# Optimization experiments

Hardware: AMD Instinct MI355X
Metric: run time of the kernel (lower is better)

The kernel has to match this reference:

```python
import jax, jax.numpy as jnp
import numpy as np

N, E, F, ED, L = 50000, 800000, 64, 16, 2
EPS_BN = 1e-5


def setup_inputs() -> dict:
    key = jax.random.key(0)
    ks = jax.random.split(key, 8)
    s = 0.05
    return {
        "x": jax.random.normal(ks[0], (N, F), jnp.float32),
        "edge_index": jax.random.randint(ks[1], (2, E), 0, N),
        "edge_attr": jax.random.normal(ks[2], (E, ED), jnp.float32),
        # per-layer stacked params (L layers)
        "We": jax.random.normal(ks[3], (L, ED, F), jnp.float32) * s,
        "be": jnp.zeros((L, F), jnp.float32),
        "Wpre": jax.random.normal(ks[4], (L, 2 * F, F), jnp.float32) * s,
        "bpre": jnp.zeros((L, F), jnp.float32),
        "Wpost": jax.random.normal(ks[5], (L, 7 * F, F), jnp.float32) * s,
        "bpost": jnp.zeros((L, F), jnp.float32),
        "Wlin": jax.random.normal(ks[6], (L, F, F), jnp.float32) * s,
        "blin": jnp.zeros((L, F), jnp.float32),
        "gamma": jnp.ones((L, F), jnp.float32),
        "beta": jnp.zeros((L, F), jnp.float32),
    }


def _layer(x, src, dst, edge_attr, We, be, Wpre, bpre, Wpost, bpost, Wlin, blin, gamma, beta):
    # message: edge encoder + pre-MLP on cat(x_j, e)   [E, F]
    e = edge_attr @ We + be
    h = jnp.concatenate([x[src], e], axis=-1) @ Wpre + bpre
    # multi-aggregator segment reduce to target nodes (index = dst)
    cnt = jax.ops.segment_sum(jnp.ones(h.shape[0], h.dtype), dst, num_segments=N)
    safe_cnt = jnp.maximum(cnt, 1.0)
    mean = jax.ops.segment_sum(h, dst, num_segments=N) / safe_cnt[:, None]
    empty = (cnt == 0)[:, None]
    mn = jnp.where(empty, 0.0, jax.ops.segment_min(h, dst, num_segments=N))
    mx = jnp.where(empty, 0.0, jax.ops.segment_max(h, dst, num_segments=N))
    agg = jnp.concatenate([mean, mn, mx], axis=-1)  # [N, 3F]
    # scalers: identity, then amplification (deg=None => avg from bincount of degrees)
    deg_i = cnt.astype(jnp.int32)
    bc = jnp.bincount(deg_i, length=N).astype(h.dtype)
    avg_log = jnp.mean(jnp.log(bc + 1.0))
    amp = (jnp.log(safe_cnt + 1.0) / avg_log)[:, None]
    out = jnp.concatenate([agg, agg * amp], axis=-1)  # [N, 6F]
    # post-MLP on cat(x, aggregated), final linear
    out = jnp.concatenate([x, out], axis=-1) @ Wpost + bpost  # [N, F]
    out = out @ Wlin + blin
    # BatchNorm1d (batch stats, biased var) + ReLU
    mu = out.mean(axis=0)
    var = jnp.mean((out - mu) ** 2, axis=0)
    out = gamma * (out - mu) / jnp.sqrt(var + EPS_BN) + beta
    return jax.nn.relu(out)


def reference(x, edge_index, edge_attr, We, be, Wpre, bpre, Wpost, bpost, Wlin, blin, gamma, beta):
    src, dst = edge_index[0], edge_index[1]
    for l in range(L):
        x = _layer(x, src, dst, edge_attr, We[l], be[l], Wpre[l], bpre[l],
                   Wpost[l], bpost[l], Wlin[l], blin[l], gamma[l], beta[l])
    return x
```

## Files before the change

kernel.cpp:

```cpp
#include <hip/hip_runtime.h>
#include <math.h>

static constexpr int NN = 50000;
static constexpr long NE = 800000;
static constexpr int FF = 64;
static constexpr int EDIM = 16;
static constexpr int NLAYER = 2;
static constexpr float EPSBN = 1e-5f;
static constexpr int NGRP = NN / 16;
static constexpr int SCB = 512;
static constexpr int NSCB = (NN + SCB - 1) / SCB;

typedef __attribute__((ext_vector_type(8))) short short8v;
typedef __attribute__((ext_vector_type(4))) float f32x4;

#define MFMA16(a, b, c) __builtin_amdgcn_mfma_f32_16x16x32_bf16(a, b, c, 0, 0, 0)

__device__ __forceinline__ short f2bf(float f) {
    unsigned u = __float_as_uint(f);
    unsigned r = u + 0x7FFFu + ((u >> 16) & 1u);
    return (short)(r >> 16);
}
__device__ __forceinline__ float bf2f(unsigned short h) {
    return __uint_as_float(((unsigned)h) << 16);
}
__device__ __forceinline__ unsigned pk2(float lo, float hi) {
    return (unsigned)(unsigned short)f2bf(lo) | ((unsigned)(unsigned short)f2bf(hi) << 16);
}
__device__ __forceinline__ short8v pack8(const float* p) {
    const float4* q = (const float4*)p;
    float4 a = q[0], b = q[1];
    short8v v;
    v[0] = f2bf(a.x); v[1] = f2bf(a.y); v[2] = f2bf(a.z); v[3] = f2bf(a.w);
    v[4] = f2bf(b.x); v[5] = f2bf(b.y); v[6] = f2bf(b.z); v[7] = f2bf(b.w);
    return v;
}
__device__ __forceinline__ void pack8s(const float* p, short8v& hi, short8v& lo) {
    const float4* q = (const float4*)p;
    float4 a = q[0], b = q[1];
    float v[8] = {a.x, a.y, a.z, a.w, b.x, b.y, b.z, b.w};
#pragma unroll
    for (int j = 0; j < 8; ++j) {
        short h = f2bf(v[j]);
        hi[j] = h;
        lo[j] = f2bf(v[j] - bf2f((unsigned short)h));
    }
}
__device__ __forceinline__ void pack8fs(const float* v, short8v& hi, short8v& lo) {
#pragma unroll
    for (int j = 0; j < 8; ++j) {
        short h = f2bf(v[j]);
        hi[j] = h;
        lo[j] = f2bf(v[j] - bf2f((unsigned short)h));
    }
}

__global__ void fold_kernel(const float* __restrict__ We, const float* __restrict__ be,
                            const float* __restrict__ Wpre, const float* __restrict__ bpre,
                            const float* __restrict__ Wpost, const float* __restrict__ bpost,
                            const float* __restrict__ Wlin, const float* __restrict__ blin,
                            float* __restrict__ Weff, float* __restrict__ beff,
                            float* __restrict__ Wc, float* __restrict__ cfold) {
    int l = blockIdx.x >> 4;
    int s = blockIdx.x & 15;
    int t = threadIdx.x;
    const float* We_l    = We    + l * EDIM * FF;
    const float* Wpre_e  = Wpre  + l * 2 * FF * FF + FF * FF;
    const float* Wpost_l = Wpost + l * 7 * FF * FF;
    const float* Wlin_l  = Wlin  + l * FF * FF;

    __shared__ float slin[FF * FF];
    __shared__ float spre[FF * FF];
    for (int i = t; i < FF * FF; i += blockDim.x) { slin[i] = Wlin_l[i]; spre[i] = Wpre_e[i]; }
    __syncthreads();

    for (int i = s * 256 + t; i < EDIM * FF; i += 16 * 256) {
        int j = i >> 6, f = i & 63;
        float a = 0.f;
        for (int k = 0; k < FF; ++k) a += We_l[j * FF + k] * spre[k * FF + f];
        Weff[l * EDIM * FF + i] = a;
    }
    for (int i = s * 256 + t; i < FF; i += 16 * 256) {
        float a = bpre[l * FF + i];
        for (int k = 0; k < FF; ++k) a += be[l * FF + k] * spre[k * FF + i];
        beff[l * FF + i] = a;
    }
    for (int i = s * 256 + t; i < 7 * FF * FF; i += 16 * 256) {
        int r = i >> 6, f = i & 63;
        float a = 0.f;
        for (int k = 0; k < FF; ++k) a += Wpost_l[r * FF + k] * slin[k * FF + f];
        Wc[l * 7 * FF * FF + i] = a;
    }
    for (int i = s * 256 + t; i < FF; i += 16 * 256) {
        float a = blin[l * FF + i];
        for (int k = 0; k < FF; ++k) a += bpost[l * FF + k] * slin[k * FF + i];
        cfold[l * FF + i] = a;
    }
}

__global__ void fragify_all(const float* __restrict__ Wpre, const float* __restrict__ Weff,
                            const float* __restrict__ Wc,
                            short* __restrict__ WpreF, short* __restrict__ WeffF,
                            short* __restrict__ WcFh, short* __restrict__ WcFl) {
    int b = blockIdx.x;
    int l = b / 17, r = b % 17;
    int t = threadIdx.x;
    const float* src; short* dh; short* dl = nullptr; int kc, Kreal;
    if (r < 2)      { src = Wpre + (size_t)l * 2 * FF * FF; dh = WpreF + l * 4096;  kc = r;     Kreal = 64; }
    else if (r < 3) { src = Weff + (size_t)l * EDIM * FF;   dh = WeffF + l * 2048;  kc = 0;     Kreal = 16; }
    else            { src = Wc   + (size_t)l * 7 * FF * FF; dh = WcFh + l * 28672;
                      dl = WcFl + l * 28672;                                        kc = r - 3; Kreal = 448; }
    int idx = kc * 256 + t;
    int lane = idx & 63, nt = (idx >> 6) & 3;
    int m = lane & 15, kh = lane >> 4;
    short8v hv, lv;
#pragma unroll
    for (int j = 0; j < 8; ++j) {
        int k = kc * 32 + kh * 8 + j;
        float val = (k < Kreal) ? src[k * FF + nt * 16 + m] : 0.f;
        short h = f2bf(val);
        hv[j] = h;
        lv[j] = f2bf(val - bf2f((unsigned short)h));
    }
    ((short8v*)dh)[idx] = hv;
    if (dl) ((short8v*)dl)[idx] = lv;
}


__global__ void build_zero(int* __restrict__ rowcnt, int* __restrict__ fill,
                           int* __restrict__ bc, float* __restrict__ avglog) {
    long i = (long)blockIdx.x * 256 + threadIdx.x;
    long stride = (long)gridDim.x * 256;
    for (long j = i; j < NN; j += stride) { rowcnt[j] = 0; fill[j] = 0; bc[j] = 0; }
    if (i == 0) avglog[0] = 0.f;
}

__global__ void hist_dst(const int* __restrict__ ei, int* __restrict__ rowcnt) {
    long e = (long)blockIdx.x * 256 + threadIdx.x;
    if (e < NE) atomicAdd(&rowcnt[ei[NE + e]], 1);
}

__global__ void scan_a(const int* __restrict__ rowcnt, int* __restrict__ part) {
    __shared__ int red[SCB];
    int t = threadIdx.x;
    int i = blockIdx.x * SCB + t;
    red[t] = (i < NN) ? rowcnt[i] : 0;
    __syncthreads();
    for (int o = SCB / 2; o > 0; o >>= 1) {
        if (t < o) red[t] += red[t + o];
        __syncthreads();
    }
    if (t == 0) part[blockIdx.x] = red[0];
}

__global__ void scan_b(int* __restrict__ part, int* __restrict__ rowptr) {
    __shared__ int s[128];
    int t = threadIdx.x;
    int v = (t < NSCB) ? part[t] : 0;
    s[t] = v;
    __syncthreads();
    for (int o = 1; o < 128; o <<= 1) {
        int u = (t >= o) ? s[t - o] : 0;
        __syncthreads();
        s[t] += u;
        __syncthreads();
    }
    if (t < NSCB) part[t] = s[t] - v;
    if (t == 127) rowptr[NN] = s[127];
}

__global__ void scan_c(const int* __restrict__ rowcnt, const int* __restrict__ part,
                       int* __restrict__ rowptr) {
    __shared__ int s[SCB];
    int t = threadIdx.x;
    int i = blockIdx.x * SCB + t;
    int v = (i < NN) ? rowcnt[i] : 0;
    s[t] = v;
    __syncthreads();
    for (int o = 1; o < SCB; o <<= 1) {
        int u = (t >= o) ? s[t - o] : 0;
        __syncthreads();
        s[t] += u;
        __syncthreads();
    }
    if (i < NN) rowptr[i] = part[blockIdx.x] + s[t] - v;
}

__global__ void scatter_perm(const int* __restrict__ ei, const int* __restrict__ rowptr,
                             int* __restrict__ fill, int2* __restrict__ srcperm) {
    long e = (long)blockIdx.x * 256 + threadIdx.x;
    if (e >= NE) return;
    int d = ei[NE + e];
    int p = rowptr[d] + atomicAdd(&fill[d], 1);
    srcperm[p] = make_int2(ei[e], (int)e);
}

__global__ void gather_attr(const int2* __restrict__ srcperm, const float* __restrict__ attr,
                            int* __restrict__ srcp, short* __restrict__ attrb) {
    long p = (long)blockIdx.x * 256 + threadIdx.x;
    if (p >= NE) return;
    int2 sp = srcperm[p];
    srcp[p] = sp.x;
    long e = sp.y;
    const float4* a4 = (const float4*)(attr + e * EDIM);
    float4 A = a4[0], B = a4[1], C = a4[2], D = a4[3];
    uint4 w0, w1;
    w0.x = pk2(A.x, A.y); w0.y = pk2(A.z, A.w); w0.z = pk2(B.x, B.y); w0.w = pk2(B.z, B.w);
    w1.x = pk2(C.x, C.y); w1.y = pk2(C.z, C.w); w1.z = pk2(D.x, D.y); w1.w = pk2(D.z, D.w);
    uint4* dst = (uint4*)(attrb + p * EDIM);
    dst[0] = w0; dst[1] = w1;
}

__global__ void degbc2(const int* __restrict__ rowcnt, int* __restrict__ bc) {
    __shared__ int h[256];
    int t = threadIdx.x;
    h[t] = 0;
    __syncthreads();
    for (long n = (long)blockIdx.x * 256 + t; n < NN; n += (long)gridDim.x * 256) {
        int d = rowcnt[n];
        if (d < 256) {
            atomicAdd(&h[d], 1);
        } else {
            if (d >= NN) d = NN - 1;
            atomicAdd(&bc[d], 1);
        }
    }
    __syncthreads();
    int v = h[t];
    if (v) atomicAdd(&bc[t], v);
}

__global__ void avglog_kernel(const int* __restrict__ bc, float* __restrict__ total) {
    float s = 0.f;
    for (long i = (long)blockIdx.x * 256 + threadIdx.x; i < NN; i += (long)gridDim.x * 256)
        s += logf((float)bc[i] + 1.f);
    for (int o = 32; o; o >>= 1) s += __shfl_down(s, o, 64);
    __shared__ float wsum[4];
    int lane = threadIdx.x & 63, wid = threadIdx.x >> 6;
    if (lane == 0) wsum[wid] = s;
    __syncthreads();
    if (threadIdx.x == 0) atomicAdd(total, wsum[0] + wsum[1] + wsum[2] + wsum[3]);
}

__global__ void amp_kernel(const int* __restrict__ cnt, const float* __restrict__ total,
                           float* __restrict__ amp) {
    long n = (long)blockIdx.x * 256 + threadIdx.x;
    if (n < NN) {
        float avg = total[0] / (float)NN;
        float sc = fmaxf((float)cnt[n], 1.f);
        amp[n] = logf(sc + 1.f) / avg;
    }
}


__global__ __launch_bounds__(256) void xp_mfma(const float* __restrict__ xin,
                                               const short* __restrict__ WF,
                                               short* __restrict__ xpb,
                                               float* __restrict__ bnsum,
                                               float* __restrict__ bnsum2) {
    int t = threadIdx.x;
    if (blockIdx.x == 0 && t < FF) { bnsum[t] = 0.f; bnsum2[t] = 0.f; }
    int g = blockIdx.x * 4 + (t >> 6);
    if (g >= NGRP) return;
    int lane = t & 63, m = lane & 15, kh = lane >> 4;
    const float* xr = xin + (long)(g * 16 + m) * FF;
    short8v a0 = pack8(xr + kh * 8);
    short8v a1 = pack8(xr + 32 + kh * 8);
    const short8v* BF = (const short8v*)WF;
    f32x4 acc[4];
#pragma unroll
    for (int nt = 0; nt < 4; ++nt) {
        f32x4 z = {0.f, 0.f, 0.f, 0.f};
        z = MFMA16(a0, BF[(0 * 4 + nt) * 64 + lane], z);
        z = MFMA16(a1, BF[(1 * 4 + nt) * 64 + lane], z);
        acc[nt] = z;
    }
#pragma unroll
    for (int nt = 0; nt < 4; ++nt)
#pragma unroll
        for (int r = 0; r < 4; ++r) {
            long node = g * 16 + kh * 4 + r;
            xpb[node * FF + nt * 16 + m] = f2bf(acc[nt][r]);
        }
}

__global__ __launch_bounds__(256) void ep_mfma(const short* __restrict__ attrb,
                                               const short* __restrict__ WF,
                                               const float* __restrict__ beff_l,
                                               short* __restrict__ epc, long elo) {
    int t = threadIdx.x;
    int g = blockIdx.x * 4 + (t >> 6);
    int lane = t & 63, m = lane & 15, kh = lane >> 4;
    long p0 = elo + (long)g * 16;
    short8v a;
    if (kh < 2) {
        a = *(const short8v*)(attrb + (p0 + m) * EDIM + kh * 8);
    } else {
#pragma unroll
        for (int j = 0; j < 8; ++j) a[j] = 0;
    }
    const short8v* BF = (const short8v*)WF;
    float bfv[4];
#pragma unroll
    for (int nt = 0; nt < 4; ++nt) bfv[nt] = beff_l[nt * 16 + m];
    f32x4 acc[4];
#pragma unroll
    for (int nt = 0; nt < 4; ++nt) {
        f32x4 z = {0.f, 0.f, 0.f, 0.f};
        acc[nt] = MFMA16(a, BF[nt * 64 + lane], z);
    }
#pragma unroll
    for (int nt = 0; nt < 4; ++nt)
#pragma unroll
        for (int r = 0; r < 4; ++r) {
            long rel = (long)g * 16 + kh * 4 + r;
            epc[rel * FF + nt * 16 + m] = f2bf(acc[nt][r] + bfv[nt]);
        }
}

__global__ __launch_bounds__(256) void agg_merge(
    const int* __restrict__ rowptr, const int* __restrict__ srcp,
    const short* __restrict__ xpb, const short* __restrict__ epc,
    long elo, long ehi, int first,
    float* __restrict__ sumb, float* __restrict__ mnb, float* __restrict__ mxb) {
    int t = threadIdx.x;
    int n = blockIdx.x * 4 + (t >> 6);
    if (n >= NN) return;
    int lane = t & 63;
    long r0 = rowptr[n], r1 = rowptr[n + 1];
    long lo = r0 > elo ? r0 : elo;
    long hi = r1 < ehi ? r1 : ehi;
    const float INF = __builtin_huge_valf();
    float sm = 0.f, mn = INF, mx = -INF;
    if (!first && lo >= hi) return;
    const unsigned short* xu = (const unsigned short*)xpb;
    const unsigned short* eu = (const unsigned short*)epc;
    for (long base = lo; base < hi; base += 64) {
        int cnt = (int)(((hi - base) < 64) ? (hi - base) : 64);
        int sv = srcp[base + (lane < cnt ? lane : cnt - 1)];
        long eb = base - elo;
        int j = 0;
        for (; j + 8 <= cnt; j += 8) {
            int s0 = __shfl(sv, j + 0), s1 = __shfl(sv, j + 1);
            int s2 = __shfl(sv, j + 2), s3 = __shfl(sv, j + 3);
            int s4 = __shfl(sv, j + 4), s5 = __shfl(sv, j + 5);
            int s6 = __shfl(sv, j + 6), s7 = __shfl(sv, j + 7);
            float x0 = bf2f(xu[(long)s0 * FF + lane]);
            float x1 = bf2f(xu[(long)s1 * FF + lane]);
            float x2 = bf2f(xu[(long)s2 * FF + lane]);
            float x3 = bf2f(xu[(long)s3 * FF + lane]);
            float x4 = bf2f(xu[(long)s4 * FF + lane]);
            float x5 = bf2f(xu[(long)s5 * FF + lane]);
            float x6 = bf2f(xu[(long)s6 * FF + lane]);
            float x7 = bf2f(xu[(long)s7 * FF + lane]);
            float e0 = bf2f(eu[(eb + j + 0) * FF + lane]);
            float e1 = bf2f(eu[(eb + j + 1) * FF + lane]);
            float e2 = bf2f(eu[(eb + j + 2) * FF + lane]);
            float e3 = bf2f(eu[(eb + j + 3) * FF + lane]);
            float e4 = bf2f(eu[(eb + j + 4) * FF + lane]);
            float e5 = bf2f(eu[(eb + j + 5) * FF + lane]);
            float e6 = bf2f(eu[(eb + j + 6) * FF + lane]);
            float e7 = bf2f(eu[(eb + j + 7) * FF + lane]);
            float h0 = x0 + e0, h1 = x1 + e1, h2 = x2 + e2, h3 = x3 + e3;
            float h4 = x4 + e4, h5 = x5 + e5, h6 = x6 + e6, h7 = x7 + e7;
            sm += ((h0 + h1) + (h2 + h3)) + ((h4 + h5) + (h6 + h7));
            mn = fminf(mn, fminf(fminf(fminf(h0, h1), fminf(h2, h3)),
                                 fminf(fminf(h4, h5), fminf(h6, h7))));
            mx = fmaxf(mx, fmaxf(fmaxf(fmaxf(h0, h1), fmaxf(h2, h3)),
                                 fmaxf(fmaxf(h4, h5), fmaxf(h6, h7))));
        }
        for (; j + 4 <= cnt; j += 4) {
            int s0 = __shfl(sv, j + 0), s1 = __shfl(sv, j + 1);
            int s2 = __shfl(sv, j + 2), s3 = __shfl(sv, j + 3);
            float x0 = bf2f(xu[(long)s0 * FF + lane]);
            float x1 = bf2f(xu[(long)s1 * FF + lane]);
            float x2 = bf2f(xu[(long)s2 * FF + lane]);
            float x3 = bf2f(xu[(long)s3 * FF + lane]);
            float e0 = bf2f(eu[(eb + j + 0) * FF + lane]);
            float e1 = bf2f(eu[(eb + j + 1) * FF + lane]);
            float e2 = bf2f(eu[(eb + j + 2) * FF + lane]);
            float e3 = bf2f(eu[(eb + j + 3) * FF + lane]);
            float h0 = x0 + e0, h1 = x1 + e1, h2 = x2 + e2, h3 = x3 + e3;
            sm += (h0 + h1) + (h2 + h3);
            mn = fminf(mn, fminf(fminf(h0, h1), fminf(h2, h3)));
            mx = fmaxf(mx, fmaxf(fmaxf(h0, h1), fmaxf(h2, h3)));
        }
        for (; j < cnt; ++j) {
            int s0 = __shfl(sv, j);
            float h = bf2f(xu[(long)s0 * FF + lane]) + bf2f(eu[(eb + j) * FF + lane]);
            sm += h;
            mn = fminf(mn, h);
            mx = fmaxf(mx, h);
        }
    }
    long o = (long)n * FF + lane;
    if (first) {
        sumb[o] = sm; mnb[o] = mn; mxb[o] = mx;
    } else {
        sumb[o] += sm;
        mnb[o] = fminf(mnb[o], mn);
        mxb[o] = fmaxf(mxb[o], mx);
    }
}

__global__ __launch_bounds__(256) void node_mfma(
    const float* __restrict__ xin, const float* __restrict__ sumb,
    const float* __restrict__ mnb, const float* __restrict__ mxb,
    const int* __restrict__ rowcnt, const float* __restrict__ amp,
    const short* __restrict__ WFh, const short* __restrict__ WFl,
    const float* __restrict__ cfold_l,
    float* __restrict__ out_pre, float* __restrict__ bnsum, float* __restrict__ bnsum2) {
    __shared__ float sS[FF], sQ[FF];
    int t = threadIdx.x;
    if (t < FF) { sS[t] = 0.f; sQ[t] = 0.f; }
    __syncthreads();
    int g = blockIdx.x * 4 + (t >> 6);
    bool act = (g < NGRP);
    int lane = t & 63, m = lane & 15, kh = lane >> 4;
    if (act) {
        long n = g * 16 + m;
        int deg = rowcnt[n];
        float inv = 1.f / fmaxf((float)deg, 1.f);
        bool has = (deg > 0);
        float av = amp[n];
        const float* xr = xin + n * FF;
        float vme[16], vmn[16], vmx[16], sc16[16];
        {
            const float4* s4a = (const float4*)(sumb + n * FF + kh * 8);
            const float4* s4b = (const float4*)(sumb + n * FF + 32 + kh * 8);
            float4 a = s4a[0], b = s4a[1], c = s4b[0], d = s4b[1];
            vme[0]=a.x*inv; vme[1]=a.y*inv; vme[2]=a.z*inv; vme[3]=a.w*inv;
            vme[4]=b.x*inv; vme[5]=b.y*inv; vme[6]=b.z*inv; vme[7]=b.w*inv;
            vme[8]=c.x*inv; vme[9]=c.y*inv; vme[10]=c.z*inv; vme[11]=c.w*inv;
            vme[12]=d.x*inv; vme[13]=d.y*inv; vme[14]=d.z*inv; vme[15]=d.w*inv;
        }
        {
            const float4* s4a = (const float4*)(mnb + n * FF + kh * 8);
            const float4* s4b = (const float4*)(mnb + n * FF + 32 + kh * 8);
            float4 a = s4a[0], b = s4a[1], c = s4b[0], d = s4b[1];
            vmn[0]=has?a.x:0.f; vmn[1]=has?a.y:0.f; vmn[2]=has?a.z:0.f; vmn[3]=has?a.w:0.f;
            vmn[4]=has?b.x:0.f; vmn[5]=has?b.y:0.f; vmn[6]=has?b.z:0.f; vmn[7]=has?b.w:0.f;
            vmn[8]=has?c.x:0.f; vmn[9]=has?c.y:0.f; vmn[10]=has?c.z:0.f; vmn[11]=has?c.w:0.f;
            vmn[12]=has?d.x:0.f; vmn[13]=has?d.y:0.f; vmn[14]=has?d.z:0.f; vmn[15]=has?d.w:0.f;
        }
        {
            const float4* s4a = (const float4*)(mxb + n * FF + kh * 8);
            const float4* s4b = (const float4*)(mxb + n * FF + 32 + kh * 8);
            float4 a = s4a[0], b = s4a[1], c = s4b[0], d = s4b[1];
            vmx[0]=has?a.x:0.f; vmx[1]=has?a.y:0.f; vmx[2]=has?a.z:0.f; vmx[3]=has?a.w:0.f;
            vmx[4]=has?b.x:0.f; vmx[5]=has?b.y:0.f; vmx[6]=has?b.z:0.f; vmx[7]=has?b.w:0.f;
            vmx[8]=has?c.x:0.f; vmx[9]=has?c.y:0.f; vmx[10]=has?c.z:0.f; vmx[11]=has?c.w:0.f;
            vmx[12]=has?d.x:0.f; vmx[13]=has?d.y:0.f; vmx[14]=has?d.z:0.f; vmx[15]=has?d.w:0.f;
        }
        const short8v* BH = (const short8v*)WFh;
        const short8v* BL = (const short8v*)WFl;
        f32x4 acc[4];
#pragma unroll
        for (int nt = 0; nt < 4; ++nt) { f32x4 z = {0.f,0.f,0.f,0.f}; acc[nt] = z; }
        short8v hv, lv;
#define DO_KC3(kc) { \
        _Pragma("unroll") for (int nt = 0; nt < 4; ++nt) { \
            acc[nt] = MFMA16(hv, BH[((kc) * 4 + nt) * 64 + lane], acc[nt]); \
            acc[nt] = MFMA16(lv, BH[((kc) * 4 + nt) * 64 + lane], acc[nt]); \
            acc[nt] = MFMA16(hv, BL[((kc) * 4 + nt) * 64 + lane], acc[nt]); } }
        pack8s(xr + kh * 8, hv, lv);        DO_KC3(0)
        pack8s(xr + 32 + kh * 8, hv, lv);   DO_KC3(1)
        pack8fs(vme + 0, hv, lv);           DO_KC3(2)
        pack8fs(vme + 8, hv, lv);           DO_KC3(3)
        pack8fs(vmn + 0, hv, lv);           DO_KC3(4)
        pack8fs(vmn + 8, hv, lv);           DO_KC3(5)
        pack8fs(vmx + 0, hv, lv);           DO_KC3(6)
        pack8fs(vmx + 8, hv, lv);           DO_KC3(7)
#pragma unroll
        for (int j = 0; j < 16; ++j) sc16[j] = vme[j] * av;
        pack8fs(sc16 + 0, hv, lv);          DO_KC3(8)
        pack8fs(sc16 + 8, hv, lv);          DO_KC3(9)
#pragma unroll
        for (int j = 0; j < 16; ++j) sc16[j] = vmn[j] * av;
        pack8fs(sc16 + 0, hv, lv);          DO_KC3(10)
        pack8fs(sc16 + 8, hv, lv);          DO_KC3(11)
#pragma unroll
        for (int j = 0; j < 16; ++j) sc16[j] = vmx[j] * av;
        pack8fs(sc16 + 0, hv, lv);          DO_KC3(12)
        pack8fs(sc16 + 8, hv, lv);          DO_KC3(13)
#undef DO_KC3
        float cfv[4];
#pragma unroll
        for (int nt = 0; nt < 4; ++nt) cfv[nt] = cfold_l[nt * 16 + m];
#pragma unroll
        for (int nt = 0; nt < 4; ++nt) {
            float ps = 0.f, pq = 0.f;
#pragma unroll
            for (int r = 0; r < 4; ++r) {
                float v = acc[nt][r] + cfv[nt];
                out_pre[(long)(g * 16 + kh * 4 + r) * FF + nt * 16 + m] = v;
                ps += v;
                pq += v * v;
            }
            atomicAdd(&sS[nt * 16 + m], ps);
            atomicAdd(&sQ[nt * 16 + m], pq);
        }
    }
    __syncthreads();
    if (t < FF) {
        atomicAdd(&bnsum[t], sS[t]);
        atomicAdd(&bnsum2[t], sQ[t]);
    }
}

__global__ void bn_apply2(const float* __restrict__ out_pre,
                          const float* __restrict__ bnsum, const float* __restrict__ bnsum2,
                          const float* __restrict__ gamma_l, const float* __restrict__ beta_l,
                          float* __restrict__ xout) {
    int f = threadIdx.x & 63;
    float mu = bnsum[f] / (float)NN;
    float var = bnsum2[f] / (float)NN - mu * mu;
    var = fmaxf(var, 0.f);
    float s = gamma_l[f] * rsqrtf(var + EPSBN);
    float o = beta_l[f] - mu * s;
    long i = (long)blockIdx.x * 256 + threadIdx.x;
    long stride = (long)gridDim.x * 256;
    for (long j = i; j < (long)NN * FF; j += stride) {
        xout[j] = fmaxf(fmaf(out_pre[j], s, o), 0.f);
    }
}

extern "C" void kernel_launch(void* const* d_in, const int* in_sizes, int n_in,
                              void* d_out, int out_size, void* d_ws, size_t ws_size,
                              hipStream_t stream) {
    const float* x0    = (const float*)d_in[0];
    const int*   ei    = (const int*)d_in[1];
    const float* attr  = (const float*)d_in[2];
    const float* We    = (const float*)d_in[3];
    const float* be    = (const float*)d_in[4];
    const float* Wpre  = (const float*)d_in[5];
    const float* bpre  = (const float*)d_in[6];
    const float* Wpost = (const float*)d_in[7];
    const float* bpost = (const float*)d_in[8];
    const float* Wlin  = (const float*)d_in[9];
    const float* blin  = (const float*)d_in[10];
    const float* gamma = (const float*)d_in[11];
    const float* beta  = (const float*)d_in[12];
    float* out = (float*)d_out;

    char* ws = (char*)d_ws;
    size_t off = 0;
    auto carve = [&](size_t bytes) -> void* {
        void* p = ws + off;
        off += (bytes + 255) & ~(size_t)255;
        return p;
    };
    const size_t NFb = (size_t)NN * FF * 4;
    float*    Weff   = (float*)carve(2 * EDIM * FF * 4);
    float*    beff   = (float*)carve(2 * FF * 4);
    float*    Wc     = (float*)carve(2 * 7 * FF * FF * 4);
    float*    cfold  = (float*)carve(2 * FF * 4);
    short*    WpreF  = (short*)carve(2 * 4096 * 2);
    short*    WeffF  = (short*)carve(2 * 2048 * 2);
    short*    WcFh   = (short*)carve(2 * 28672 * 2);
    short*    WcFl   = (short*)carve(2 * 28672 * 2);
    int*      srcp   = (int*)carve(NE * 4);
    short*    attrb  = (short*)carve((size_t)NE * EDIM * 2);
    int*      rowptr = (int*)carve((NN + 1) * 4);
    int*      rowcnt = (int*)carve(NN * 4);
    int*      fill   = (int*)carve(NN * 4);
    int*      bc     = (int*)carve(NN * 4);
    float*    amp    = (float*)carve(NN * 4);
    int*      part   = (int*)carve(NSCB * 4);
    short*    xpb    = (short*)carve((size_t)NN * FF * 2);
    float*    sumb   = (float*)carve(NFb);
    float*    mnb    = (float*)carve(NFb);
    float*    mxb    = (float*)carve(NFb);
    float*    xbuf   = (float*)carve(NFb);
    float*    bnsum  = (float*)carve(FF * 4);
    float*    bnsum2 = (float*)carve(FF * 4);
    float*    avglog = (float*)carve(4);
    size_t left = (ws_size > off) ? ws_size - off : 0;
    long ech = (left >= (size_t)NE * FF * 2 + 512) ? NE : NE / 2;
    short*    epc    = (short*)carve((size_t)ech * FF * 2);
    float*    out_pre = (float*)epc;
    int2*     srcperm = (int2*)xbuf;

    const int EB = (int)((NE + 255) / 256);

    build_zero<<<196, 256, 0, stream>>>(rowcnt, fill, bc, avglog);
    hist_dst<<<EB, 256, 0, stream>>>(ei, rowcnt);
    scan_a<<<NSCB, SCB, 0, stream>>>(rowcnt, part);
    scan_b<<<1, 128, 0, stream>>>(part, rowptr);
    scan_c<<<NSCB, SCB, 0, stream>>>(rowcnt, part, rowptr);
    scatter_perm<<<EB, 256, 0, stream>>>(ei, rowptr, fill, srcperm);
    gather_attr<<<EB, 256, 0, stream>>>(srcperm, attr, srcp, attrb);
    degbc2<<<196, 256, 0, stream>>>(rowcnt, bc);
    avglog_kernel<<<128, 256, 0, stream>>>(bc, avglog);
    amp_kernel<<<196, 256, 0, stream>>>(rowcnt, avglog, amp);
    fold_kernel<<<32, 256, 0, stream>>>(We, be, Wpre, bpre, Wpost, bpost, Wlin, blin,
                                        Weff, beff, Wc, cfold);
    fragify_all<<<34, 256, 0, stream>>>(Wpre, Weff, Wc, WpreF, WeffF, WcFh, WcFl);

    for (int l = 0; l < NLAYER; ++l) {
        const float* xin = (l == 0) ? x0 : xbuf;
        float* xout = (l == NLAYER - 1) ? out : xbuf;

        xp_mfma<<<(NGRP + 3) / 4, 256, 0, stream>>>(xin, WpreF + l * 4096, xpb, bnsum, bnsum2);
        for (long elo = 0; elo < NE; elo += ech) {
            ep_mfma<<<(int)(ech / 64), 256, 0, stream>>>(attrb, WeffF + l * 2048,
                                                         beff + l * FF, epc, elo);
            agg_merge<<<12500, 256, 0, stream>>>(rowptr, srcp, xpb, epc, elo, elo + ech,
                                                 (elo == 0) ? 1 : 0, sumb, mnb, mxb);
        }
        node_mfma<<<(NGRP + 3) / 4, 256, 0, stream>>>(xin, sumb, mnb, mxb, rowcnt, amp,
                                                      WcFh + l * 28672, WcFl + l * 28672,
                                                      cfold + l * FF,
                                                      out_pre, bnsum, bnsum2);
        bn_apply2<<<4096, 256, 0, stream>>>(out_pre, bnsum, bnsum2,
                                            gamma + l * FF, beta + l * FF, xout);
    }
}
```

Measured before the change: 377.0 us.

## Fuse edge-feature MFMA into aggregation kernel via per-wave LDS staging

```diff
diff --git a/kernel.cpp b/kernel.cpp
--- a/kernel.cpp
+++ b/kernel.cpp
@@ -10,6 +10,7 @@
 static constexpr int NGRP = NN / 16;
 static constexpr int SCB = 512;
 static constexpr int NSCB = (NN + SCB - 1) / SCB;
+static constexpr int LDSW = 68;
 
 typedef __attribute__((ext_vector_type(8))) short short8v;
 typedef __attribute__((ext_vector_type(4))) float f32x4;
@@ -284,61 +285,53 @@
         }
 }
 
-__global__ __launch_bounds__(256) void ep_mfma(const short* __restrict__ attrb,
-                                               const short* __restrict__ WF,
-                                               const float* __restrict__ beff_l,
-                                               short* __restrict__ epc, long elo) {
-    int t = threadIdx.x;
-    int g = blockIdx.x * 4 + (t >> 6);
-    int lane = t & 63, m = lane & 15, kh = lane >> 4;
-    long p0 = elo + (long)g * 16;
-    short8v a;
-    if (kh < 2) {
-        a = *(const short8v*)(attrb + (p0 + m) * EDIM + kh * 8);
-    } else {
-#pragma unroll
-        for (int j = 0; j < 8; ++j) a[j] = 0;
-    }
+__global__ __launch_bounds__(256) void agg_fused(
+    const int* __restrict__ rowptr, const int* __restrict__ srcp,
+    const short* __restrict__ attrb, const short* __restrict__ WF,
+    const float* __restrict__ beff_l, const short* __restrict__ xpb,
+    float* __restrict__ sumb, float* __restrict__ mnb, float* __restrict__ mxb) {
+    __shared__ float eph[4][16 * LDSW];
+    int t = threadIdx.x;
+    int wid = t >> 6, lane = t & 63;
+    int m = lane & 15, kh = lane >> 4;
+    int n = blockIdx.x * 4 + wid;
+    if (n >= NN) return;
+    float* lds = &eph[wid][0];
     const short8v* BF = (const short8v*)WF;
     float bfv[4];
 #pragma unroll
     for (int nt = 0; nt < 4; ++nt) bfv[nt] = beff_l[nt * 16 + m];
-    f32x4 acc[4];
-#pragma unroll
-    for (int nt = 0; nt < 4; ++nt) {
-        f32x4 z = {0.f, 0.f, 0.f, 0.f};
-        acc[nt] = MFMA16(a, BF[nt * 64 + lane], z);
-    }
-#pragma unroll
-    for (int nt = 0; nt < 4; ++nt)
-#pragma unroll
-        for (int r = 0; r < 4; ++r) {
-            long rel = (long)g * 16 + kh * 4 + r;
-            epc[rel * FF + nt * 16 + m] = f2bf(acc[nt][r] + bfv[nt]);
-        }
-}
-
-__global__ __launch_bounds__(256) void agg_merge(
-    const int* __restrict__ rowptr, const int* __restrict__ srcp,
-    const short* __restrict__ xpb, const short* __restrict__ epc,
-    long elo, long ehi, int first,
-    float* __restrict__ sumb, float* __restrict__ mnb, float* __restrict__ mxb) {
-    int t = threadIdx.x;
-    int n = blockIdx.x * 4 + (t >> 6);
-    if (n >= NN) return;
-    int lane = t & 63;
     long r0 = rowptr[n], r1 = rowptr[n + 1];
-    long lo = r0 > elo ? r0 : elo;
-    long hi = r1 < ehi ? r1 : ehi;
     const float INF = __builtin_huge_valf();
     float sm = 0.f, mn = INF, mx = -INF;
-    if (!first && lo >= hi) return;
     const unsigned short* xu = (const unsigned short*)xpb;
-    const unsigned short* eu = (const unsigned short*)epc;
-    for (long base = lo; base < hi; base += 64) {
-        int cnt = (int)(((hi - base) < 64) ? (hi - base) : 64);
+
+    for (long base = r0; base < r1; base += 16) {
+        int cnt = (int)(((r1 - base) < 16) ? (r1 - base) : 16);
+        long ea = base + m; if (ea > NE - 1) ea = NE - 1;
+        short8v a;
+        if (kh < 2) {
+            a = *(const short8v*)(attrb + ea * EDIM + kh * 8);
+        } else {
+#pragma unroll
+            for (int j = 0; j < 8; ++j) a[j] = 0;
+        }
+        f32x4 ac0, ac1, ac2, ac3;
+        {
+            f32x4 z = {0.f, 0.f, 0.f, 0.f};
+            ac0 = MFMA16(a, BF[0 * 64 + lane], z);
+            ac1 = MFMA16(a, BF[1 * 64 + lane], z);
+            ac2 = MFMA16(a, BF[2 * 64 + lane], z);
+            ac3 = MFMA16(a, BF[3 * 64 + lane], z);
+        }
+#pragma unroll
+        for (int r = 0; r < 4; ++r) {
+            lds[(kh * 4 + r) * LDSW + 0 * 16 + m] = ac0[r] + bfv[0];
+            lds[(kh * 4 + r) * LDSW + 1 * 16 + m] = ac1[r] + bfv[1];
+            lds[(kh * 4 + r) * LDSW + 2 * 16 + m] = ac2[r] + bfv[2];
+            lds[(kh * 4 + r) * LDSW + 3 * 16 + m] = ac3[r] + bfv[3];
+        }
         int sv = srcp[base + (lane < cnt ? lane : cnt - 1)];
-        long eb = base - elo;
         int j = 0;
         for (; j + 8 <= cnt; j += 8) {
             int s0 = __shfl(sv, j + 0), s1 = __shfl(sv, j + 1);
@@ -353,54 +346,30 @@
             float x5 = bf2f(xu[(long)s5 * FF + lane]);
             float x6 = bf2f(xu[(long)s6 * FF + lane]);
             float x7 = bf2f(xu[(long)s7 * FF + lane]);
-            float e0 = bf2f(eu[(eb + j + 0) * FF + lane]);
-            float e1 = bf2f(eu[(eb + j + 1) * FF + lane]);
-            float e2 = bf2f(eu[(eb + j + 2) * FF + lane]);
-            float e3 = bf2f(eu[(eb + j + 3) * FF + lane]);
-            float e4 = bf2f(eu[(eb + j + 4) * FF + lane]);
-            float e5 = bf2f(eu[(eb + j + 5) * FF + lane]);
-            float e6 = bf2f(eu[(eb + j + 6) * FF + lane]);
-            float e7 = bf2f(eu[(eb + j + 7) * FF + lane]);
-            float h0 = x0 + e0, h1 = x1 + e1, h2 = x2 + e2, h3 = x3 + e3;
-            float h4 = x4 + e4, h5 = x5 + e5, h6 = x6 + e6, h7 = x7 + e7;
+            float h0 = x0 + lds[(j + 0) * LDSW + lane];
+            float h1 = x1 + lds[(j + 1) * LDSW + lane];
+            float h2 = x2 + lds[(j + 2) * LDSW + lane];
+            float h3 = x3 + lds[(j + 3) * LDSW + lane];
+            float h4 = x4 + lds[(j + 4) * LDSW + lane];
+            float h5 = x5 + lds[(j + 5) * LDSW + lane];
+            float h6 = x6 + lds[(j + 6) * LDSW + lane];
+            float h7 = x7 + lds[(j + 7) * LDSW + lane];
             sm += ((h0 + h1) + (h2 + h3)) + ((h4 + h5) + (h6 + h7));
             mn = fminf(mn, fminf(fminf(fminf(h0, h1), fminf(h2, h3)),
                                  fminf(fminf(h4, h5), fminf(h6, h7))));
             mx = fmaxf(mx, fmaxf(fmaxf(fmaxf(h0, h1), fmaxf(h2, h3)),
                                  fmaxf(fmaxf(h4, h5), fmaxf(h6, h7))));
         }
-        for (; j + 4 <= cnt; j += 4) {
-            int s0 = __shfl(sv, j + 0), s1 = __shfl(sv, j + 1);
-            int s2 = __shfl(sv, j + 2), s3 = __shfl(sv, j + 3);
-            float x0 = bf2f(xu[(long)s0 * FF + lane]);
-            float x1 = bf2f(xu[(long)s1 * FF + lane]);
-            float x2 = bf2f(xu[(long)s2 * FF + lane]);
-            float x3 = bf2f(xu[(long)s3 * FF + lane]);
-            float e0 = bf2f(eu[(eb + j + 0) * FF + lane]);
-            float e1 = bf2f(eu[(eb + j + 1) * FF + lane]);
-            float e2 = bf2f(eu[(eb + j + 2) * FF + lane]);
-            float e3 = bf2f(eu[(eb + j + 3) * FF + lane]);
-            float h0 = x0 + e0, h1 = x1 + e1, h2 = x2 + e2, h3 = x3 + e3;
-            sm += (h0 + h1) + (h2 + h3);
-            mn = fminf(mn, fminf(fminf(h0, h1), fminf(h2, h3)));
-            mx = fmaxf(mx, fmaxf(fmaxf(h0, h1), fmaxf(h2, h3)));
-        }
         for (; j < cnt; ++j) {
             int s0 = __shfl(sv, j);
-            float h = bf2f(xu[(long)s0 * FF + lane]) + bf2f(eu[(eb + j) * FF + lane]);
+            float h = bf2f(xu[(long)s0 * FF + lane]) + lds[j * LDSW + lane];
             sm += h;
             mn = fminf(mn, h);
             mx = fmaxf(mx, h);
         }
     }
     long o = (long)n * FF + lane;
-    if (first) {
-        sumb[o] = sm; mnb[o] = mn; mxb[o] = mx;
-    } else {
-        sumb[o] += sm;
-        mnb[o] = fminf(mnb[o], mn);
-        mxb[o] = fmaxf(mxb[o], mx);
-    }
+    sumb[o] = sm; mnb[o] = mn; mxb[o] = mx;
 }
 
 __global__ __launch_bounds__(256) void node_mfma(
@@ -572,13 +541,10 @@
     float*    mnb    = (float*)carve(NFb);
     float*    mxb    = (float*)carve(NFb);
     float*    xbuf   = (float*)carve(NFb);
+    float*    out_pre = (float*)carve(NFb);
     float*    bnsum  = (float*)carve(FF * 4);
     float*    bnsum2 = (float*)carve(FF * 4);
     float*    avglog = (float*)carve(4);
-    size_t left = (ws_size > off) ? ws_size - off : 0;
-    long ech = (left >= (size_t)NE * FF * 2 + 512) ? NE : NE / 2;
-    short*    epc    = (short*)carve((size_t)ech * FF * 2);
-    float*    out_pre = (float*)epc;
     int2*     srcperm = (int2*)xbuf;
 
     const int EB = (int)((NE + 255) / 256);
@@ -602,12 +568,8 @@
         float* xout = (l == NLAYER - 1) ? out : xbuf;
 
         xp_mfma<<<(NGRP + 3) / 4, 256, 0, stream>>>(xin, WpreF + l * 4096, xpb, bnsum, bnsum2);
-        for (long elo = 0; elo < NE; elo += ech) {
-            ep_mfma<<<(int)(ech / 64), 256, 0, stream>>>(attrb, WeffF + l * 2048,
-                                                         beff + l * FF, epc, elo);
-            agg_merge<<<12500, 256, 0, stream>>>(rowptr, srcp, xpb, epc, elo, elo + ech,
-                                                 (elo == 0) ? 1 : 0, sumb, mnb, mxb);
-        }
+        agg_fused<<<12500, 256, 0, stream>>>(rowptr, srcp, attrb, WeffF + l * 2048,
+                                             beff + l * FF, xpb, sumb, mnb, mxb);
         node_mfma<<<(NGRP + 3) / 4, 256, 0, stream>>>(xin, sumb, mnb, mxb, rowcnt, amp,
                                                       WcFh + l * 28672, WcFl + l * 28672,
                                                       cfold + l * FF,
```

Result: faster. 348.5 us (-7.6%).
